# Optimization experiments

Hardware: AMD Instinct MI355X
Metric: run time of the kernel (lower is better)

## Reference

```python
import jax, jax.numpy as jnp
import numpy as np

CEN_WEIGHT = 0.5
EPS = 1e-10


def setup_inputs() -> dict:
    key = jax.random.key(0)
    k1, k2, k3 = jax.random.split(key, 3)
    num_mods, N, B = 2, 500000, 100
    logits = jax.random.normal(k1, (num_mods, N, B), dtype=jnp.float32)
    preds = jax.nn.softmax(logits, axis=-1)  # module expects probability bins
    labs = jax.random.randint(k2, (num_mods, N), 0, B).astype(jnp.int64)
    cen_in = jax.random.randint(k3, (num_mods, N), 0, 2).astype(jnp.int32)
    return {"preds": preds, "labs": labs, "cen_in": cen_in}


def _mod_loss(p, lab, cen, labs0):
    # p: [N, B] probabilities; lab: [N] bin labels for this mod;
    # cen: [N] censor flags; labs0: [N] times from mod 0 (as in original code)
    N, B = p.shape
    uncen_mask = (cen == 0)
    cen_mask = (cen == 1)
    num_uncen = jnp.sum(uncen_mask).astype(p.dtype)
    num_cen = jnp.sum(cen_mask).astype(p.dtype)

    # uncensored: -mean log p[i, lab_i]
    g = jnp.take_along_axis(p, lab[:, None].astype(jnp.int32), axis=1)[:, 0]
    uncen_loss = -jnp.sum(jnp.where(uncen_mask, jnp.log(g + EPS), 0.0)) \
        / jnp.maximum(1.0, num_uncen)

    # censored: -log(sum_{j > t_i} p[i, j]); suffix-sum replaces the python
    # loop over unique times (grouped sums of per-example terms are identical)
    suffix = jnp.flip(jnp.cumsum(jnp.flip(p, axis=1), axis=1), axis=1)  # sum_{j>=k}
    suffix = jnp.concatenate([suffix, jnp.zeros((N, 1), p.dtype)], axis=1)
    t1 = (labs0 + 1)[:, None].astype(jnp.int32)
    s = jnp.take_along_axis(suffix, t1, axis=1)[:, 0]
    cen_loss = jnp.sum(jnp.where(cen_mask, -jnp.log(s + EPS), 0.0)) \
        / jnp.maximum(1.0, num_cen)

    n = jnp.asarray(N, p.dtype)
    return (num_uncen / n) * uncen_loss + (num_cen / n) * cen_loss * CEN_WEIGHT


def reference(preds, labs, cen_in):
    labs0 = labs[0]
    losses = jax.vmap(_mod_loss, in_axes=(0, 0, 0, None))(preds, labs, cen_in, labs0)
    return jnp.sum(losses)
```

## Files before the change

kernel.cpp:

```cpp
#include <hip/hip_runtime.h>
#include <hip/hip_bf16.h>


#define HSL_EPS 1e-10f
#define NBLK 2048

__global__ __launch_bounds__(256, 8) void hsl_main(
    const float* __restrict__ preds,
    const int*   __restrict__ labs,
    const int*   __restrict__ cen,
    double*       __restrict__ bsums,
    unsigned int* __restrict__ bcnts,
    long long N)
{
    const long long R = 2LL * N;
    const int q = threadIdx.x & 3;
    const long long g0 = ((long long)blockIdx.x * blockDim.x + threadIdx.x) >> 2;
    const long long ng = ((long long)gridDim.x * blockDim.x) >> 2;

    double usum[2] = {0.0, 0.0};
    double csum[2] = {0.0, 0.0};
    unsigned int ucnt[2] = {0u, 0u};
    unsigned int ccnt[2] = {0u, 0u};

    for (long long r = g0; r < R; r += ng) {
        const int m = (r >= N) ? 1 : 0;
        const long long i0 = r - (long long)m * N;
        const int c   = cen[r];
        const int lab = labs[r];
        const int t1  = labs[i0] + 1;

        const int lo = (c == 0) ? lab : t1;
        const int hi = (c == 0) ? lab : 99;

        const float4* rowp4 = (const float4*)(preds + r * 100);

        float acc = 0.0f;
        #pragma unroll
        for (int k = 0; k < 7; ++k) {
            const int f4 = 4 * k + q;
            if (f4 < 25) {
                const float4 v = rowp4[f4];
                const int j0 = 4 * f4;
                #pragma unroll
                for (int e = 0; e < 4; ++e) {
                    const int j = j0 + e;
                    const float p = ((const float*)&v)[e];
                    acc += (j >= lo && j <= hi) ? p : 0.0f;
                }
            }
        }

        acc += __shfl_xor(acc, 1, 64);
        acc += __shfl_xor(acc, 2, 64);

        if (q == 0) {
            const double lg = (double)logf(acc + HSL_EPS);
            if (c == 0) { usum[m] += lg; ucnt[m]++; }
            else        { csum[m] += lg; ccnt[m]++; }
        }
    }

    #pragma unroll
    for (int off = 32; off > 0; off >>= 1) {
        usum[0] += __shfl_down(usum[0], off, 64);
        csum[0] += __shfl_down(csum[0], off, 64);
        usum[1] += __shfl_down(usum[1], off, 64);
        csum[1] += __shfl_down(csum[1], off, 64);
        ucnt[0] += __shfl_down(ucnt[0], off, 64);
        ccnt[0] += __shfl_down(ccnt[0], off, 64);
        ucnt[1] += __shfl_down(ucnt[1], off, 64);
        ccnt[1] += __shfl_down(ccnt[1], off, 64);
    }

    __shared__ double sh_sums[4][4];
    __shared__ unsigned int sh_cnts[4][4];
    const int waveInBlk = threadIdx.x >> 6;
    const int lane = threadIdx.x & 63;
    if (lane == 0) {
        sh_sums[waveInBlk][0] = usum[0]; sh_sums[waveInBlk][1] = csum[0];
        sh_sums[waveInBlk][2] = usum[1]; sh_sums[waveInBlk][3] = csum[1];
        sh_cnts[waveInBlk][0] = ucnt[0]; sh_cnts[waveInBlk][1] = ccnt[0];
        sh_cnts[waveInBlk][2] = ucnt[1]; sh_cnts[waveInBlk][3] = ccnt[1];
    }
    __syncthreads();
    if (threadIdx.x < 4) {
        const int slot = threadIdx.x;
        double s = 0.0; unsigned int k = 0u;
        for (int w = 0; w < 4; ++w) { s += sh_sums[w][slot]; k += sh_cnts[w][slot]; }
        bsums[slot * NBLK + blockIdx.x] = s;
        bcnts[slot * NBLK + blockIdx.x] = k;
    }
}

__global__ __launch_bounds__(256) void hsl_final(
    const double* __restrict__ bsums,
    const unsigned int* __restrict__ bcnts,
    float* __restrict__ out, long long N, int nblk)
{
    double s[4] = {0.0, 0.0, 0.0, 0.0};
    double kc[4] = {0.0, 0.0, 0.0, 0.0};
    for (int b = threadIdx.x; b < nblk; b += 256) {
        #pragma unroll
        for (int slot = 0; slot < 4; ++slot) {
            s[slot]  += bsums[slot * nblk + b];
            kc[slot] += (double)bcnts[slot * nblk + b];
        }
    }

    #pragma unroll
    for (int off = 32; off > 0; off >>= 1) {
        #pragma unroll
        for (int slot = 0; slot < 4; ++slot) {
            s[slot]  += __shfl_down(s[slot],  off, 64);
            kc[slot] += __shfl_down(kc[slot], off, 64);
        }
    }

    __shared__ double sh[4][8];
    const int waveInBlk = threadIdx.x >> 6;
    const int lane = threadIdx.x & 63;
    if (lane == 0) {
        #pragma unroll
        for (int slot = 0; slot < 4; ++slot) {
            sh[waveInBlk][slot]     = s[slot];
            sh[waveInBlk][4 + slot] = kc[slot];
        }
    }
    __syncthreads();
    if (threadIdx.x == 0) {
        double fs[4], fk[4];
        #pragma unroll
        for (int slot = 0; slot < 4; ++slot) {
            fs[slot] = sh[0][slot] + sh[1][slot] + sh[2][slot] + sh[3][slot];
            fk[slot] = sh[0][4+slot] + sh[1][4+slot] + sh[2][4+slot] + sh[3][4+slot];
        }
        float total = 0.0f;
        const float n = (float)N;
        for (int m = 0; m < 2; ++m) {
            const float nu = (float)fk[2 * m + 0];
            const float nc = (float)fk[2 * m + 1];
            const float us = (float)fs[2 * m + 0];
            const float cs = (float)fs[2 * m + 1];
            const float uncen_loss = -us / fmaxf(1.0f, nu);
            const float cen_loss   = -cs / fmaxf(1.0f, nc);
            total += (nu / n) * uncen_loss + (nc / n) * cen_loss * 0.5f;
        }
        out[0] = total;
    }
}

extern "C" void kernel_launch(void* const* d_in, const int* in_sizes, int n_in,
                              void* d_out, int out_size, void* d_ws, size_t ws_size,
                              hipStream_t stream)
{
    const float* preds = (const float*)d_in[0];
    const int*   labs  = (const int*)d_in[1];
    const int*   cen   = (const int*)d_in[2];
    float* out = (float*)d_out;

    const long long N = (long long)(in_sizes[1] / 2);

    double*       bsums = (double*)d_ws;
    unsigned int* bcnts = (unsigned int*)((char*)d_ws + (size_t)4 * NBLK * sizeof(double));

    hsl_main<<<NBLK, 256, 0, stream>>>(preds, labs, cen, bsums, bcnts, N);
    hsl_final<<<1, 256, 0, stream>>>(bsums, bcnts, out, N, NBLK);
}
```

Before: 565.9 us.

## Tile rows per block with fully coalesced float4 loads and LDS partial sums

Replaces the per-row quad-of-threads scheme with block tiles of 256 rows. Each tile is read as one contiguous float4 stream, so every thread loads consecutive memory. Masked partial sums go into shared memory and are then reduced per row by one thread. Row metadata (lo/hi/censor) is staged in LDS. The aim is fully coalesced streaming of the 400MB input. The cost is three barriers per tile, about 25KB of LDS per block, lower occupancy (launch bounds drop to 4 blocks), and a per-element integer divide.

```diff
diff --git a/kernel.cpp b/kernel.cpp
--- a/kernel.cpp
+++ b/kernel.cpp
@@ -4,8 +4,10 @@
 
 #define HSL_EPS 1e-10f
 #define NBLK 2048
-
-__global__ __launch_bounds__(256, 8) void hsl_main(
+#define TILE 256
+#define F4R  25
+
+__global__ __launch_bounds__(256, 4) void hsl_main(
     const float* __restrict__ preds,
     const int*   __restrict__ labs,
     const int*   __restrict__ cen,
@@ -14,51 +16,80 @@
     long long N)
 {
     const long long R = 2LL * N;
-    const int q = threadIdx.x & 3;
-    const long long g0 = ((long long)blockIdx.x * blockDim.x + threadIdx.x) >> 2;
-    const long long ng = ((long long)gridDim.x * blockDim.x) >> 2;
+    const long long ntiles = (R + TILE - 1) / TILE;
+    const int t = threadIdx.x;
 
     double usum[2] = {0.0, 0.0};
     double csum[2] = {0.0, 0.0};
     unsigned int ucnt[2] = {0u, 0u};
     unsigned int ccnt[2] = {0u, 0u};
 
-    for (long long r = g0; r < R; r += ng) {
-        const int m = (r >= N) ? 1 : 0;
-        const long long i0 = r - (long long)m * N;
-        const int c   = cen[r];
-        const int lab = labs[r];
-        const int t1  = labs[i0] + 1;
-
-        const int lo = (c == 0) ? lab : t1;
-        const int hi = (c == 0) ? lab : 99;
-
-        const float4* rowp4 = (const float4*)(preds + r * 100);
-
-        float acc = 0.0f;
-        #pragma unroll
-        for (int k = 0; k < 7; ++k) {
-            const int f4 = 4 * k + q;
-            if (f4 < 25) {
-                const float4 v = rowp4[f4];
-                const int j0 = 4 * f4;
-                #pragma unroll
-                for (int e = 0; e < 4; ++e) {
-                    const int j = j0 + e;
-                    const float p = ((const float*)&v)[e];
-                    acc += (j >= lo && j <= hi) ? p : 0.0f;
-                }
+    __shared__ int   sh_lo[TILE];
+    __shared__ int   sh_hi[TILE];
+    __shared__ int   sh_c [TILE];
+    __shared__ float sh_part[TILE * F4R];
+
+    for (long long tb = blockIdx.x; tb < ntiles; tb += gridDim.x) {
+        const long long r0 = tb * (long long)TILE;
+        const int nrow = (int)((R - r0 < (long long)TILE) ? (R - r0) : (long long)TILE);
+
+        if (t < nrow) {
+            const long long r = r0 + t;
+            const int c    = cen[r];
+            const int lab  = labs[r];
+            const int lab0 = (r >= N) ? labs[r - N] : lab;
+            sh_c[t]  = c;
+            sh_lo[t] = c ? (lab0 + 1) : lab;
+            sh_hi[t] = c ? 99 : lab;
+        }
+        __syncthreads();
+
+        const float4* tp4 = (const float4*)(preds + r0 * 100);
+        if (nrow == TILE) {
+            #pragma unroll 5
+            for (int it = 0; it < F4R; ++it) {
+                const int f = t + it * 256;
+                const float4 v = tp4[f];
+                const unsigned row = (unsigned)f / (unsigned)F4R;
+                const int j0 = (f - (int)row * F4R) * 4;
+                const int lo = sh_lo[row];
+                const int hi = sh_hi[row];
+                float s = 0.0f;
+                s += (j0     >= lo && j0     <= hi) ? v.x : 0.0f;
+                s += (j0 + 1 >= lo && j0 + 1 <= hi) ? v.y : 0.0f;
+                s += (j0 + 2 >= lo && j0 + 2 <= hi) ? v.z : 0.0f;
+                s += (j0 + 3 >= lo && j0 + 3 <= hi) ? v.w : 0.0f;
+                sh_part[f] = s;
             }
-        }
-
-        acc += __shfl_xor(acc, 1, 64);
-        acc += __shfl_xor(acc, 2, 64);
-
-        if (q == 0) {
-            const double lg = (double)logf(acc + HSL_EPS);
-            if (c == 0) { usum[m] += lg; ucnt[m]++; }
-            else        { csum[m] += lg; ccnt[m]++; }
-        }
+        } else {
+            const int nf4 = nrow * F4R;
+            for (int f = t; f < nf4; f += 256) {
+                const float4 v = tp4[f];
+                const unsigned row = (unsigned)f / (unsigned)F4R;
+                const int j0 = (f - (int)row * F4R) * 4;
+                const int lo = sh_lo[row];
+                const int hi = sh_hi[row];
+                float s = 0.0f;
+                s += (j0     >= lo && j0     <= hi) ? v.x : 0.0f;
+                s += (j0 + 1 >= lo && j0 + 1 <= hi) ? v.y : 0.0f;
+                s += (j0 + 2 >= lo && j0 + 2 <= hi) ? v.z : 0.0f;
+                s += (j0 + 3 >= lo && j0 + 3 <= hi) ? v.w : 0.0f;
+                sh_part[f] = s;
+            }
+        }
+        __syncthreads();
+
+        if (t < nrow) {
+            float sum = 0.0f;
+            #pragma unroll
+            for (int k = 0; k < F4R; ++k) sum += sh_part[t * F4R + k];
+            const long long r = r0 + t;
+            const int m = (r >= N) ? 1 : 0;
+            const double lg = (double)logf(sum + HSL_EPS);
+            if (sh_c[t] == 0) { usum[m] += lg; ucnt[m]++; }
+            else              { csum[m] += lg; ccnt[m]++; }
+        }
+        __syncthreads();
     }
 
     #pragma unroll
```

Measured after the change: 525.5 us. 7.1% less time.

## Read only needed float4 span per row, using complement for short prefixes

Applied to the files above, without the earlier changes.

Each thread now processes a whole row by itself instead of four threads sharing a row. For uncensored rows it loads only the single float4 holding the label bin. For censored rows it loads only the shorter side of the split, computing the tail sum as one minus the prefix when the prefix is shorter. This is meant to cut memory traffic on the preds tensor, which dominates the cost. In exchange, accesses become scattered per lane and uncoalesced, and the 1-acc complement assumes each row sums to exactly one, which adds float rounding error. The grid is also doubled to 4096 blocks.

```diff
diff --git a/kernel.cpp b/kernel.cpp
--- a/kernel.cpp
+++ b/kernel.cpp
@@ -3,7 +3,7 @@
 
 
 #define HSL_EPS 1e-10f
-#define NBLK 2048
+#define NBLK 4096
 
 __global__ __launch_bounds__(256, 8) void hsl_main(
     const float* __restrict__ preds,
@@ -14,48 +14,52 @@
     long long N)
 {
     const long long R = 2LL * N;
-    const int q = threadIdx.x & 3;
-    const long long g0 = ((long long)blockIdx.x * blockDim.x + threadIdx.x) >> 2;
-    const long long ng = ((long long)gridDim.x * blockDim.x) >> 2;
+    const int lane = threadIdx.x & 63;
+    const long long w0 = ((long long)blockIdx.x * blockDim.x + threadIdx.x) >> 6;
+    const long long nw = ((long long)gridDim.x * blockDim.x) >> 6;
 
     double usum[2] = {0.0, 0.0};
     double csum[2] = {0.0, 0.0};
     unsigned int ucnt[2] = {0u, 0u};
     unsigned int ccnt[2] = {0u, 0u};
 
-    for (long long r = g0; r < R; r += ng) {
-        const int m = (r >= N) ? 1 : 0;
-        const long long i0 = r - (long long)m * N;
-        const int c   = cen[r];
-        const int lab = labs[r];
-        const int t1  = labs[i0] + 1;
+    for (long long rb = w0 * 64; rb < R; rb += nw * 64) {
+        const long long r = rb + lane;
+        const bool valid = (r < R);
+        const long long rc = valid ? r : (R - 1);
 
-        const int lo = (c == 0) ? lab : t1;
-        const int hi = (c == 0) ? lab : 99;
+        const int m    = (rc >= N) ? 1 : 0;
+        const int c    = cen[rc];
+        const int lab  = labs[rc];
+        const int lab0 = m ? labs[rc - N] : lab;
+        const int t1   = lab0 + 1;
 
-        const float4* rowp4 = (const float4*)(preds + r * 100);
+        int lo, hi; bool flip = false;
+        if (c == 0)        { lo = lab; hi = lab; }
+        else if (t1 <= 50) { lo = 0;   hi = t1 - 1; flip = true; }
+        else               { lo = t1;  hi = 99; }
+        const int s4 = lo >> 2;
+        const int e4 = hi >> 2;
+
+        const float4* rowp4 = (const float4*)(preds + rc * 100);
 
         float acc = 0.0f;
         #pragma unroll
-        for (int k = 0; k < 7; ++k) {
-            const int f4 = 4 * k + q;
-            if (f4 < 25) {
+        for (int k = 0; k < 13; ++k) {
+            const int f4 = s4 + k;
+            if (f4 <= e4) {
                 const float4 v = rowp4[f4];
                 const int j0 = 4 * f4;
-                #pragma unroll
-                for (int e = 0; e < 4; ++e) {
-                    const int j = j0 + e;
-                    const float p = ((const float*)&v)[e];
-                    acc += (j >= lo && j <= hi) ? p : 0.0f;
-                }
+                acc += (j0     >= lo && j0     <= hi) ? v.x : 0.0f;
+                acc += (j0 + 1 >= lo && j0 + 1 <= hi) ? v.y : 0.0f;
+                acc += (j0 + 2 >= lo && j0 + 2 <= hi) ? v.z : 0.0f;
+                acc += (j0 + 3 >= lo && j0 + 3 <= hi) ? v.w : 0.0f;
             }
         }
 
-        acc += __shfl_xor(acc, 1, 64);
-        acc += __shfl_xor(acc, 2, 64);
-
-        if (q == 0) {
-            const double lg = (double)logf(acc + HSL_EPS);
+        if (valid) {
+            const float s = flip ? (1.0f - acc) : acc;
+            const double lg = (double)logf(s + HSL_EPS);
             if (c == 0) { usum[m] += lg; ucnt[m]++; }
             else        { csum[m] += lg; ccnt[m]++; }
         }
@@ -76,7 +80,6 @@
     __shared__ double sh_sums[4][4];
     __shared__ unsigned int sh_cnts[4][4];
     const int waveInBlk = threadIdx.x >> 6;
-    const int lane = threadIdx.x & 63;
     if (lane == 0) {
         sh_sums[waveInBlk][0] = usum[0]; sh_sums[waveInBlk][1] = csum[0];
         sh_sums[waveInBlk][2] = usum[1]; sh_sums[waveInBlk][3] = csum[1];
```

After: 495.4 us. -12.5%, faster.
